# Kernel optimization log

Hardware: AMD Instinct MI355X
Metric: run time of the kernel (lower is better)

Reference implementation:

```python
import jax, jax.numpy as jnp
import numpy as np

NUM_HEAD = 8


def setup_inputs() -> dict:
    key = jax.random.key(0)
    k1, k2, k3 = jax.random.split(key, 3)
    B, C, H, W = 8, 512, 32, 32
    x = jax.random.normal(k1, (B, C, H, W), dtype=jnp.float32)
    # 1x1 conv weights stored as plain matrices (out_ch, in_ch)
    Wqkv = jax.random.normal(k2, (3 * C, C), dtype=jnp.float32) * (1.0 / np.sqrt(C))
    Wo = jax.random.normal(k3, (C, C), dtype=jnp.float32) * (1.0 / np.sqrt(C))
    bo = jnp.zeros((C,), dtype=jnp.float32)
    return {"x": x, "Wqkv": Wqkv, "Wo": Wo, "bo": bo}


def reference(x, Wqkv, Wo, bo):
    B, C, H, W = x.shape
    nh = NUM_HEAD
    d = C // nh
    S = H * W
    scale = 1.0 / np.sqrt(d)
    # 1x1 conv == channel matmul: (B,3C,H,W)
    x_ = jnp.einsum('bchw,oc->bohw', x, Wqkv)
    # reshape to (B, nh, 3d, H, W) and chunk along dim 2 (matches torch chunk order)
    qkv = x_.reshape(B, nh, 3 * d, H, W)
    q, k, v = qkv[:, :, :d], qkv[:, :, d:2 * d], qkv[:, :, 2 * d:]
    # flatten heads into batch, spatial into sequence
    q = q.reshape(B * nh, d, S).transpose(0, 2, 1) * scale  # (BH, S, d)
    k = k.reshape(B * nh, d, S)                             # (BH, d, S)
    v = v.reshape(B * nh, d, S).transpose(0, 2, 1)          # (BH, S, d)
    attn = jax.nn.softmax(jnp.matmul(q, k), axis=-1)        # (BH, S, S)
    out = jnp.matmul(attn, v)                               # (BH, S, d)
    result = out.transpose(0, 2, 1).reshape(B, C, H, W)
    # output 1x1 conv with bias + residual
    y = jnp.einsum('bchw,oc->bohw', result, Wo) + bo[None, :, None, None]
    return y + x
```

## Files before the change

### kernel.cpp

```cpp
#include <hip/hip_runtime.h>
#include <hip/hip_bf16.h>

#define C_DIM 512
#define S_DIM 1024
#define NH 8
#define HD 64

typedef __attribute__((ext_vector_type(8))) short bf16x8;
typedef __attribute__((ext_vector_type(8))) unsigned short u16x8;
typedef __attribute__((ext_vector_type(4))) unsigned short u16x4;
typedef __attribute__((ext_vector_type(4))) float f32x4;

__device__ __forceinline__ unsigned short f2b_hw(float f) {
  __hip_bfloat16 h = __float2bfloat16(f);
  return __builtin_bit_cast(unsigned short, h);
}

__device__ __forceinline__ f32x4 mfma16(bf16x8 a, bf16x8 b, f32x4 c) {
  return __builtin_amdgcn_mfma_f32_16x16x32_bf16(a, b, c, 0, 0, 0);
}

__device__ __forceinline__ void gload_lds16(const unsigned short* g, unsigned short* l) {
  __builtin_amdgcn_global_load_lds(
      (const __attribute__((address_space(1))) unsigned int*)g,
      (__attribute__((address_space(3))) unsigned int*)l, 16, 0, 0);
}

__global__ __launch_bounds__(256) void prep(
    const float* __restrict__ x, const float* __restrict__ Wqkv,
    const float* __restrict__ Wo,
    unsigned short* __restrict__ WqkvB, unsigned short* __restrict__ WoB,
    unsigned short* __restrict__ xT)
{
  __shared__ float T[64][65];
  const int bid = blockIdx.x;
  if (bid < 1024) {
    const int i = bid * 256 + threadIdx.x;
    const float* src;
    unsigned short* dst;
    int off;
    float mul = 1.0f;
    if (i < 196608) {
      src = Wqkv; dst = WqkvB; off = i * 4;
      const int o = off >> 9;
      if ((o % 192) < 64) mul = 0.18033688011112042f;
    } else {
      src = Wo; dst = WoB; off = (i - 196608) * 4;
    }
    const float4 v = *(const float4*)(src + off);
    const u16x4 pk = {f2b_hw(v.x * mul), f2b_hw(v.y * mul),
                      f2b_hw(v.z * mul), f2b_hw(v.w * mul)};
    *(u16x4*)(dst + off) = pk;
  } else {
    const int idx = bid - 1024;
    const int st = idx & 15, ct = (idx >> 4) & 7, b = idx >> 7;
    const int c0 = ct * 64, s0 = st * 64;
    const int tr = threadIdx.x >> 4, tc4 = (threadIdx.x & 15) * 4;
#pragma unroll
    for (int rep = 0; rep < 4; ++rep) {
      const int c = rep * 16 + tr;
      *(float4*)&T[c][tc4] =
          *(const float4*)(x + ((size_t)(b * C_DIM + c0 + c)) * S_DIM + s0 + tc4);
    }
    __syncthreads();
#pragma unroll
    for (int rep = 0; rep < 4; ++rep) {
      const int s = rep * 16 + tr;
      const u16x4 pk = {f2b_hw(T[tc4 + 0][s]), f2b_hw(T[tc4 + 1][s]),
                        f2b_hw(T[tc4 + 2][s]), f2b_hw(T[tc4 + 3][s])};
      *(u16x4*)(xT + ((size_t)(b * S_DIM + s0 + s)) * C_DIM + c0 + tc4) = pk;
    }
  }
}

template <int MODE>
__global__ __launch_bounds__(256) void mfma_proj(
    const unsigned short* __restrict__ A, const unsigned short* __restrict__ Bm,
    unsigned short* __restrict__ Q, unsigned short* __restrict__ K,
    unsigned short* __restrict__ Vt,
    float* __restrict__ y, const float* __restrict__ bo,
    const float* __restrict__ resid)
{
  const int b = blockIdx.z, ot = blockIdx.y, st = blockIdx.x;
  const int o0 = ot * 128, s0 = st * 128;
  const int tid = threadIdx.x;
  const int w = tid >> 6, lane = tid & 63;
  const int g = lane >> 4, j16 = lane & 15;
  const int wr = w >> 1, wc = w & 1;

  __shared__ __align__(16) unsigned short lds[2048 * 8];
  char* const Al = (char*)lds;
  char* const Bl = (char*)lds + 16384;

  f32x4 acc[4][4];
#pragma unroll
  for (int mt = 0; mt < 4; ++mt)
#pragma unroll
    for (int nt = 0; nt < 4; ++nt) {
      acc[mt][nt].x = 0.f; acc[mt][nt].y = 0.f;
      acc[mt][nt].z = 0.f; acc[mt][nt].w = 0.f;
    }

  for (int k0 = 0; k0 < C_DIM; k0 += 64) {
    __syncthreads();
#pragma unroll
    for (int it = 0; it < 8; ++it) {
      const int chunk = it * 256 + tid;
      const int cid = chunk & 1023;
      const int row = cid >> 3;
      const int colb = (cid & 7) << 4;
      const int srcb = colb ^ ((row & 7) << 4);
      const unsigned short* gp;
      if (it < 4) gp = A + (size_t)(o0 + row) * C_DIM + k0 + (srcb >> 1);
      else        gp = Bm + ((size_t)(b * S_DIM) + s0 + row) * C_DIM + k0 + (srcb >> 1);
      gload_lds16(gp, lds + (size_t)(it * 256 + w * 64) * 8);
    }
    __syncthreads();

#pragma unroll
    for (int ks = 0; ks < 2; ++ks) {
      bf16x8 af[4], bfr[4];
#pragma unroll
      for (int mt = 0; mt < 4; ++mt) {
        const int r = wr * 64 + mt * 16 + j16;
        af[mt] = __builtin_bit_cast(
            bf16x8, *(const u16x8*)(Al + r * 128 + ((ks * 64 + g * 16) ^ ((r & 7) << 4))));
      }
#pragma unroll
      for (int nt = 0; nt < 4; ++nt) {
        const int r = wc * 64 + nt * 16 + j16;
        bfr[nt] = __builtin_bit_cast(
            bf16x8, *(const u16x8*)(Bl + r * 128 + ((ks * 64 + g * 16) ^ ((r & 7) << 4))));
      }
#pragma unroll
      for (int mt = 0; mt < 4; ++mt)
#pragma unroll
        for (int nt = 0; nt < 4; ++nt)
          acc[mt][nt] = mfma16(af[mt], bfr[nt], acc[mt][nt]);
    }
  }

#pragma unroll
  for (int mt = 0; mt < 4; ++mt) {
    const int ob = o0 + wr * 64 + mt * 16 + g * 4;
    if (MODE == 0) {
      const int head = ob / 192, type = (ob % 192) >> 6, d = ob & 63;
      const int bh = b * NH + head;
      if (type < 2) {
        unsigned short* const dst = (type == 0) ? Q : K;
#pragma unroll
        for (int nt = 0; nt < 4; ++nt) {
          const int s = s0 + wc * 64 + nt * 16 + j16;
          const f32x4 a = acc[mt][nt];
          const u16x4 pk = {f2b_hw(a.x), f2b_hw(a.y), f2b_hw(a.z), f2b_hw(a.w)};
          *(u16x4*)(dst + ((size_t)bh * S_DIM + s) * HD + d) = pk;
        }
      } else {
#pragma unroll
        for (int nt = 0; nt < 4; ++nt) {
          const int spos = nt * 16 + j16;
          const int p = (spos & 35) | ((spos & 12) << 1) | ((spos & 16) >> 2);
          const size_t col = (size_t)(s0 + wc * 64 + p);
          const f32x4 a = acc[mt][nt];
#pragma unroll
          for (int q = 0; q < 4; ++q)
            Vt[((size_t)bh * HD + d + q) * S_DIM + col] = f2b_hw(a[q]);
        }
      }
    } else {
#pragma unroll
      for (int nt = 0; nt < 4; ++nt) {
        const int s = s0 + wc * 64 + nt * 16 + j16;
#pragma unroll
        for (int q = 0; q < 4; ++q) {
          const int o = ob + q;
          const size_t idx = ((size_t)(b * C_DIM + o)) * S_DIM + s;
          y[idx] = acc[mt][nt][q] + bo[o] + resid[idx];
        }
      }
    }
  }
}

__global__ __launch_bounds__(256) void attn_mfma(
    const unsigned short* __restrict__ Qg, const unsigned short* __restrict__ Kg,
    const unsigned short* __restrict__ Vg, unsigned short* __restrict__ AOt)
{
  const int bh = blockIdx.x;
  const int qb = blockIdx.y;
  const int b = bh >> 3, head = bh & 7;
  const int tid = threadIdx.x;
  const int w = tid >> 6, lane = tid & 63;
  const int g = lane >> 4, j16 = lane & 15;
  const int qw0 = qb * 128 + w * 32;

  __shared__ __align__(16) unsigned short KV[3][2][4096];

  bf16x8 qf[2][2];
#pragma unroll
  for (int nt = 0; nt < 2; ++nt)
#pragma unroll
    for (int ks = 0; ks < 2; ++ks)
      qf[nt][ks] = __builtin_bit_cast(
          bf16x8, *(const u16x8*)(Qg + ((size_t)bh * S_DIM + qw0 + nt * 16 + j16) * HD +
                                  ks * 32 + g * 8));

  auto STAGE = [&](int buf, int k0) {
#pragma unroll
    for (int it = 0; it < 2; ++it) {
      const int cid = tid + it * 256;
      const int row = cid >> 3;
      const int srcb = ((cid & 7) << 4) ^ ((row & 7) << 4);
      unsigned short* const dst = &KV[buf][0][0] + (size_t)(it * 256 + w * 64) * 8;
      gload_lds16(Kg + ((size_t)bh * S_DIM + k0 + row) * HD + (srcb >> 1), dst);
      gload_lds16(Vg + ((size_t)bh * HD + row) * S_DIM + k0 + (srcb >> 1), dst + 4096);
    }
  };

  f32x4 oacc[4][2];
#pragma unroll
  for (int mt = 0; mt < 4; ++mt)
#pragma unroll
    for (int nt = 0; nt < 2; ++nt) {
      oacc[mt][nt].x = 0.f; oacc[mt][nt].y = 0.f;
      oacc[mt][nt].z = 0.f; oacc[mt][nt].w = 0.f;
    }
  float lsum[2] = {0.f, 0.f};

  STAGE(0, 0);
  STAGE(1, 64);

  for (int kt = 0; kt < 16; ++kt) {
    if (kt < 15) asm volatile("s_waitcnt vmcnt(4)" ::: "memory");
    else         asm volatile("s_waitcnt vmcnt(0)" ::: "memory");
    __builtin_amdgcn_s_barrier();
    if (kt < 14) STAGE((kt + 2) % 3, (kt + 2) * 64);

    const char* const Kl = (const char*)KV + (kt % 3) * 16384;
    const char* const Vl = Kl + 8192;

    f32x4 sacc[4][2];
    __builtin_amdgcn_s_setprio(1);
#pragma unroll
    for (int mt = 0; mt < 4; ++mt) {
      const int row = mt * 16 + j16;
      const int sw = (row & 7) << 4;
#pragma unroll
      for (int ks = 0; ks < 2; ++ks) {
        const bf16x8 kf = __builtin_bit_cast(
            bf16x8, *(const u16x8*)(Kl + row * 128 + ((ks * 64 + g * 16) ^ sw)));
        if (ks == 0) {
#pragma unroll
          for (int nt = 0; nt < 2; ++nt) {
            f32x4 z; z.x = 0.f; z.y = 0.f; z.z = 0.f; z.w = 0.f;
            sacc[mt][nt] = mfma16(kf, qf[nt][0], z);
          }
        } else {
#pragma unroll
          for (int nt = 0; nt < 2; ++nt)
            sacc[mt][nt] = mfma16(kf, qf[nt][1], sacc[mt][nt]);
        }
      }
    }
    __builtin_amdgcn_s_setprio(0);

    u16x4 pf4[2][4];
#pragma unroll
    for (int mt = 0; mt < 4; ++mt)
#pragma unroll
      for (int nt = 0; nt < 2; ++nt) {
        f32x4 p;
        p.x = exp2f(sacc[mt][nt].x);
        p.y = exp2f(sacc[mt][nt].y);
        p.z = exp2f(sacc[mt][nt].z);
        p.w = exp2f(sacc[mt][nt].w);
        lsum[nt] += (p.x + p.y) + (p.z + p.w);
        pf4[nt][mt] = u16x4{f2b_hw(p.x), f2b_hw(p.y), f2b_hw(p.z), f2b_hw(p.w)};
      }

    __builtin_amdgcn_s_setprio(1);
#pragma unroll
    for (int ks = 0; ks < 2; ++ks) {
      bf16x8 pfr[2];
#pragma unroll
      for (int nt = 0; nt < 2; ++nt)
        pfr[nt] = __builtin_bit_cast(
            bf16x8, __builtin_shufflevector(pf4[nt][2 * ks], pf4[nt][2 * ks + 1],
                                            0, 1, 2, 3, 4, 5, 6, 7));
#pragma unroll
      for (int mt = 0; mt < 4; ++mt) {
        const int row = mt * 16 + j16;
        const int sw = (row & 7) << 4;
        const bf16x8 vf = __builtin_bit_cast(
            bf16x8, *(const u16x8*)(Vl + row * 128 + ((ks * 64 + g * 16) ^ sw)));
#pragma unroll
        for (int nt = 0; nt < 2; ++nt)
          oacc[mt][nt] = mfma16(vf, pfr[nt], oacc[mt][nt]);
      }
    }
    __builtin_amdgcn_s_setprio(0);
  }

#pragma unroll
  for (int nt = 0; nt < 2; ++nt) {
    lsum[nt] += __shfl_xor(lsum[nt], 16);
    lsum[nt] += __shfl_xor(lsum[nt], 32);
    lsum[nt] = 1.f / lsum[nt];
  }

#pragma unroll
  for (int mt = 0; mt < 4; ++mt)
#pragma unroll
    for (int nt = 0; nt < 2; ++nt) {
      const int q = qw0 + nt * 16 + j16;
      const f32x4 a = oacc[mt][nt];
      const float rl = lsum[nt];
      const u16x4 pk = {f2b_hw(a.x * rl), f2b_hw(a.y * rl), f2b_hw(a.z * rl), f2b_hw(a.w * rl)};
      *(u16x4*)(AOt + ((size_t)(b * S_DIM + q)) * C_DIM + head * HD + mt * 16 + g * 4) = pk;
    }
}

extern "C" void kernel_launch(void* const* d_in, const int* in_sizes, int n_in,
                              void* d_out, int out_size, void* d_ws, size_t ws_size,
                              hipStream_t stream) {
  const float* x    = (const float*)d_in[0];
  const float* Wqkv = (const float*)d_in[1];
  const float* Wo   = (const float*)d_in[2];
  const float* bo   = (const float*)d_in[3];
  float* y = (float*)d_out;

  unsigned short* WqkvB = (unsigned short*)d_ws;
  unsigned short* WoB   = WqkvB + 786432;
  unsigned short* xT    = WoB + 262144;
  unsigned short* Q     = xT + 4194304;
  unsigned short* K     = Q + 4194304;
  unsigned short* Vt    = K + 4194304;
  unsigned short* AOt   = Vt + 4194304;

  prep<<<dim3(2048), 256, 0, stream>>>(x, Wqkv, Wo, WqkvB, WoB, xT);
  mfma_proj<0><<<dim3(8, 12, 8), 256, 0, stream>>>(WqkvB, xT, Q, K, Vt,
                                                   nullptr, nullptr, nullptr);
  attn_mfma<<<dim3(64, 8), 256, 0, stream>>>(Q, K, Vt, AOt);
  mfma_proj<1><<<dim3(8, 4, 8), 256, 0, stream>>>(WoB, AOt, nullptr, nullptr, nullptr,
                                                  y, bo, x);
}
```

Baseline: 81.95 us.

## Software-pipeline QK^T of next tile with softmax and PV of current tile

Restructures the attention inner loop so the QK^T MFMAs for tile i+1 are issued while the exp/convert and PV MFMAs of tile i run, using ping-pong score register arrays. The loop is manually unrolled by two, and barriers and waitcnt placement are reordered around the staging of the next K/V tile. The goal is to hide transcendental and conversion latency behind matrix work. In exchange it adds register pressure from the second score buffer and an extra barrier per iteration.

```diff
diff --git a/kernel.cpp b/kernel.cpp
--- a/kernel.cpp
+++ b/kernel.cpp
@@ -217,6 +217,27 @@
     }
   };
 
+  auto QKT = [&](int KT, f32x4 (&SACC)[4][2]) {
+    const char* const Kl = (const char*)KV + (KT % 3) * 16384;
+#pragma unroll
+    for (int mt = 0; mt < 4; ++mt) {
+      const int row = mt * 16 + j16;
+      const int sw = (row & 7) << 4;
+      const bf16x8 kf0 = __builtin_bit_cast(
+          bf16x8, *(const u16x8*)(Kl + row * 128 + ((g * 16) ^ sw)));
+#pragma unroll
+      for (int nt = 0; nt < 2; ++nt) {
+        f32x4 z; z.x = 0.f; z.y = 0.f; z.z = 0.f; z.w = 0.f;
+        SACC[mt][nt] = mfma16(kf0, qf[nt][0], z);
+      }
+      const bf16x8 kf1 = __builtin_bit_cast(
+          bf16x8, *(const u16x8*)(Kl + row * 128 + ((64 + g * 16) ^ sw)));
+#pragma unroll
+      for (int nt = 0; nt < 2; ++nt)
+        SACC[mt][nt] = mfma16(kf1, qf[nt][1], SACC[mt][nt]);
+    }
+  };
+
   f32x4 oacc[4][2];
 #pragma unroll
   for (int mt = 0; mt < 4; ++mt)
@@ -227,79 +248,69 @@
     }
   float lsum[2] = {0.f, 0.f};
 
+  f32x4 sA[4][2], sB[4][2];
+
   STAGE(0, 0);
   STAGE(1, 64);
-
-  for (int kt = 0; kt < 16; ++kt) {
-    if (kt < 15) asm volatile("s_waitcnt vmcnt(4)" ::: "memory");
-    else         asm volatile("s_waitcnt vmcnt(0)" ::: "memory");
-    __builtin_amdgcn_s_barrier();
-    if (kt < 14) STAGE((kt + 2) % 3, (kt + 2) * 64);
-
-    const char* const Kl = (const char*)KV + (kt % 3) * 16384;
-    const char* const Vl = Kl + 8192;
-
-    f32x4 sacc[4][2];
-    __builtin_amdgcn_s_setprio(1);
-#pragma unroll
-    for (int mt = 0; mt < 4; ++mt) {
-      const int row = mt * 16 + j16;
-      const int sw = (row & 7) << 4;
-#pragma unroll
-      for (int ks = 0; ks < 2; ++ks) {
-        const bf16x8 kf = __builtin_bit_cast(
-            bf16x8, *(const u16x8*)(Kl + row * 128 + ((ks * 64 + g * 16) ^ sw)));
-        if (ks == 0) {
-#pragma unroll
-          for (int nt = 0; nt < 2; ++nt) {
-            f32x4 z; z.x = 0.f; z.y = 0.f; z.z = 0.f; z.w = 0.f;
-            sacc[mt][nt] = mfma16(kf, qf[nt][0], z);
-          }
-        } else {
-#pragma unroll
-          for (int nt = 0; nt < 2; ++nt)
-            sacc[mt][nt] = mfma16(kf, qf[nt][1], sacc[mt][nt]);
-        }
-      }
-    }
-    __builtin_amdgcn_s_setprio(0);
-
-    u16x4 pf4[2][4];
-#pragma unroll
-    for (int mt = 0; mt < 4; ++mt)
-#pragma unroll
-      for (int nt = 0; nt < 2; ++nt) {
-        f32x4 p;
-        p.x = exp2f(sacc[mt][nt].x);
-        p.y = exp2f(sacc[mt][nt].y);
-        p.z = exp2f(sacc[mt][nt].z);
-        p.w = exp2f(sacc[mt][nt].w);
-        lsum[nt] += (p.x + p.y) + (p.z + p.w);
-        pf4[nt][mt] = u16x4{f2b_hw(p.x), f2b_hw(p.y), f2b_hw(p.z), f2b_hw(p.w)};
-      }
-
-    __builtin_amdgcn_s_setprio(1);
-#pragma unroll
-    for (int ks = 0; ks < 2; ++ks) {
-      bf16x8 pfr[2];
-#pragma unroll
-      for (int nt = 0; nt < 2; ++nt)
-        pfr[nt] = __builtin_bit_cast(
-            bf16x8, __builtin_shufflevector(pf4[nt][2 * ks], pf4[nt][2 * ks + 1],
-                                            0, 1, 2, 3, 4, 5, 6, 7));
-#pragma unroll
-      for (int mt = 0; mt < 4; ++mt) {
-        const int row = mt * 16 + j16;
-        const int sw = (row & 7) << 4;
-        const bf16x8 vf = __builtin_bit_cast(
-            bf16x8, *(const u16x8*)(Vl + row * 128 + ((ks * 64 + g * 16) ^ sw)));
-#pragma unroll
-        for (int nt = 0; nt < 2; ++nt)
-          oacc[mt][nt] = mfma16(vf, pfr[nt], oacc[mt][nt]);
-      }
-    }
-    __builtin_amdgcn_s_setprio(0);
-  }
+  asm volatile("s_waitcnt vmcnt(4)" ::: "memory");
+  __builtin_amdgcn_s_barrier();
+  QKT(0, sA);
+
+#define ATTN_BODY(I, SCUR, SNXT)                                               \
+  {                                                                            \
+                      \
+    u16x4 pf4[2][4];                                                           \
+    _Pragma("unroll")                                                          \
+    for (int mt = 0; mt < 4; ++mt)                                             \
+      _Pragma("unroll")                                                        \
+      for (int nt = 0; nt < 2; ++nt) {                                         \
+        f32x4 p;                                                               \
+        p.x = exp2f(SCUR[mt][nt].x);                                           \
+        p.y = exp2f(SCUR[mt][nt].y);                                           \
+        p.z = exp2f(SCUR[mt][nt].z);                                           \
+        p.w = exp2f(SCUR[mt][nt].w);                                           \
+        lsum[nt] += (p.x + p.y) + (p.z + p.w);                                 \
+        pf4[nt][mt] = u16x4{f2b_hw(p.x), f2b_hw(p.y), f2b_hw(p.z), f2b_hw(p.w)}; \
+      }                                                                        \
+    __builtin_amdgcn_s_barrier();   \
+    if ((I) < 14) STAGE(((I) + 2) % 3, ((I) + 2) * 64);                        \
+    if ((I) < 14)      asm volatile("s_waitcnt vmcnt(4)" ::: "memory");        \
+    else if ((I) == 14) asm volatile("s_waitcnt vmcnt(0)" ::: "memory");       \
+    if ((I) < 15) __builtin_amdgcn_s_barrier();    \
+    __builtin_amdgcn_s_setprio(1);                                             \
+    if ((I) < 15) QKT((I) + 1, SNXT);      \
+    {                                                                          \
+      const char* const Vl = (const char*)KV + ((I) % 3) * 16384 + 8192;       \
+      _Pragma("unroll")                                                        \
+      for (int ks = 0; ks < 2; ++ks) {                                         \
+        bf16x8 pfr[2];                                                         \
+        _Pragma("unroll")                                                      \
+        for (int nt = 0; nt < 2; ++nt)                                         \
+          pfr[nt] = __builtin_bit_cast(                                        \
+              bf16x8, __builtin_shufflevector(pf4[nt][2 * ks],                 \
+                                              pf4[nt][2 * ks + 1],             \
+                                              0, 1, 2, 3, 4, 5, 6, 7));        \
+        _Pragma("unroll")                                                      \
+        for (int mt = 0; mt < 4; ++mt) {                                       \
+          const int row = mt * 16 + j16;                                       \
+          const int sw = (row & 7) << 4;                                       \
+          const bf16x8 vf = __builtin_bit_cast(                                \
+              bf16x8, *(const u16x8*)(Vl + row * 128 + ((ks * 64 + g * 16) ^ sw))); \
+          _Pragma("unroll")                                                    \
+          for (int nt = 0; nt < 2; ++nt)                                       \
+            oacc[mt][nt] = mfma16(vf, pfr[nt], oacc[mt][nt]);                  \
+        }                                                                      \
+      }                                                                        \
+    }                                                                          \
+    __builtin_amdgcn_s_setprio(0);                                             \
+  }
+
+#pragma unroll
+  for (int ii = 0; ii < 8; ++ii) {
+    ATTN_BODY(2 * ii,     sA, sB)
+    ATTN_BODY(2 * ii + 1, sB, sA)
+  }
+#undef ATTN_BODY
 
 #pragma unroll
   for (int nt = 0; nt < 2; ++nt) {
```

New measurement: 111.6 us. 1.36x slower.
